# Kernel tuning notes

Hardware: AMD Instinct MI355X
Metric: run time of the kernel (lower is better)

Reference implementation:

```python
import jax, jax.numpy as jnp
import numpy as np

DIM, HID, SEQ = 768, 2048, 4096
LR, MOM, WD, THRESH = 1e-3, 0.9, 0.01, 0.1


def _net(p, x):
    W1, b1, W2, b2, W3, b3, W4, b4 = p
    h = jax.nn.relu(x @ W1 + b1)
    h = jax.nn.relu(h @ W2 + b2)
    h = jax.nn.relu(h @ W3 + b3)
    return h @ W4 + b4


def _loss(p, t):
    # t: [dim]; token.unsqueeze(0) then mse_loss (mean over all elements)
    pred = _net(p, t[None, :])
    return jnp.mean((pred - t[None, :]) ** 2)


def _ttt(params, x):
    toks = x[::4]  # `if i % 4 != 0: continue`

    def step(carry, t):
        p, buf, inited = carry
        g = jax.grad(_loss)(p, t)
        surprise = sum(jnp.linalg.norm(gi) for gi in jax.tree_util.tree_leaves(g))
        # momentum buffer: first observation initializes it
        buf_new = jnp.where(inited, MOM * buf + (1.0 - MOM) * surprise, surprise)

        def upd(q):
            qd = jax.tree_util.tree_map(lambda w: w * (1.0 - WD), q)  # weight decay
            g2 = jax.grad(_loss)(qd, t)                                # fresh fwd/bwd
            return jax.tree_util.tree_map(lambda w, gi: w - LR * gi, qd, g2)  # SGD step

        p_new = jax.lax.cond(buf_new > THRESH, upd, lambda q: q, p)
        return (p_new, buf_new, jnp.bool_(True)), None

    (pf, _, _), _ = jax.lax.scan(step, (params, jnp.float32(0.0), jnp.bool_(False)), toks)
    return pf


def setup_inputs() -> dict:
    key = jax.random.key(0)
    ks = jax.random.split(key, 5)

    def lin(k, fi, fo):
        kw, kb = jax.random.split(k)
        w = jax.random.normal(kw, (fi, fo), jnp.float32) / np.sqrt(fi).astype(np.float32)
        b = jax.random.normal(kb, (fo,), jnp.float32) * 0.01
        return w, b

    W1, b1 = lin(ks[0], DIM, HID)
    W2, b2 = lin(ks[1], HID, HID)
    W3, b3 = lin(ks[2], HID, HID)
    W4, b4 = lin(ks[3], HID, DIM)
    x = jax.random.normal(ks[4], (SEQ, DIM), jnp.float32)
    return dict(x=x, W1=W1, b1=b1, W2=W2, b2=b2, W3=W3, b3=b3, W4=W4, b4=b4, do_ttt=1)


def reference(x, W1, b1, W2, b2, W3, b3, W4, b4, do_ttt):
    params = (W1, b1, W2, b2, W3, b3, W4, b4)
    if do_ttt:
        params = _ttt(params, x)
    out = _net(params, x)            # eval pass over full sequence
    return out.mean(axis=0, keepdims=True)  # memory_summary [1, dim]
```

## Files before the change

### kernel.cpp

```cpp
#include <hip/hip_runtime.h>
#include <cstddef>

#define LRC 0.001f
#define DEC 0.99f

static const size_t OFF_Z1P = 0;
static const size_t OFF_Z2P = 65536;
static const size_t OFF_Z2Q = 131072;
static const size_t OFF_Z3P = 196608;
static const size_t OFF_Z3Q = 262144;
static const size_t OFF_Z4P = 327680;
static const size_t OFF_Z4Q = 352256;
static const size_t OFF_H1F = 376832;
static const size_t OFF_H1Q = 378880;
static const size_t OFF_H2F = 380928;
static const size_t OFF_H2Q = 382976;
static const size_t OFF_H3F = 385024;
static const size_t OFF_H3Q = 387072;
static const size_t OFF_D4F = 389120;
static const size_t OFF_D4Q = 389888;
static const size_t OFF_D3F = 390656;
static const size_t OFF_D3Q = 392704;
static const size_t OFF_D2F = 394752;
static const size_t OFF_D2Q = 396800;
static const size_t OFF_D1F = 398848;
static const size_t OFF_D1Q = 400896;
static const size_t OFF_NSQ = 402944;
static const size_t OFF_SL3 = 402960;
static const size_t OFF_SL2 = 403216;
static const size_t OFF_SL1 = 403472;
static const size_t OFF_BUF = 403728;
static const size_t OFF_MSUM = 403732;
static const size_t OFF_HA  = 428308;
static const size_t OFF_HB  = 2525460;

__device__ inline void fma4(float4& a, float s, const float4& w) {
    a.x += s * w.x; a.y += s * w.y; a.z += s * w.z; a.w += s * w.w;
}

__device__ float block_reduce_512(float v) {
    __shared__ float red[512];
    int t = threadIdx.x;
    red[t] = v;
    __syncthreads();
    for (int s = 256; s > 0; s >>= 1) {
        if (t < s) red[t] += red[t + s];
        __syncthreads();
    }
    float r = red[0];
    __syncthreads();
    return r;
}

__global__ __launch_bounds__(512) void k_fwd1(const float* __restrict__ xt,
                                              const float* __restrict__ W1,
                                              float* __restrict__ z1p,
                                              const int* __restrict__ flag) {
    if (*flag == 0) return;
    int b = blockIdx.x;
    int g = b >> 5, p = b & 31;
    int tid = threadIdx.x, w = tid >> 6, lane = tid & 63;
    int c0 = g * 256 + lane * 4;
    int kb = p * 24 + w * 3;
    float4 acc = make_float4(0.f, 0.f, 0.f, 0.f);
#pragma unroll
    for (int r = 0; r < 3; ++r) {
        float a = xt[kb + r];
        const float4 wv = *(const float4*)(W1 + (size_t)(kb + r) * 2048 + c0);
        fma4(acc, a, wv);
    }
    __shared__ float4 red[8][64];
    red[w][lane] = acc;
    __syncthreads();
    if (w == 0) {
        float4 s = red[0][lane];
#pragma unroll
        for (int q = 1; q < 8; ++q) {
            float4 r2 = red[q][lane];
            s.x += r2.x; s.y += r2.y; s.z += r2.z; s.w += r2.w;
        }
        *(float4*)(z1p + (size_t)p * 2048 + c0) = s;
    }
}

__global__ __launch_bounds__(512) void k_fwd2(const float* __restrict__ zinP,
                                              const float* __restrict__ zinQ,
                                              const float* __restrict__ bin,
                                              const float* __restrict__ W, int Nout,
                                              float* __restrict__ zoutP,
                                              float* __restrict__ zoutQ,
                                              const int* __restrict__ flag) {
    if (*flag == 0) return;
    int b = blockIdx.x;
    int g = b >> 5, p = b & 31;
    int tid = threadIdx.x, w = tid >> 6, lane = tid & 63;
    __shared__ float hs[64], hq[64];
    if (tid < 64) {
        int k = p * 64 + tid;
        float s = 0.f;
#pragma unroll 8
        for (int pp = 0; pp < 32; ++pp) s += zinP[pp * 2048 + k];
        float bv = bin[k];
        float h = fmaxf(s + bv, 0.f);
        float hqq;
        if (zinQ) {
            float sq = 0.f;
#pragma unroll 8
            for (int pp = 0; pp < 32; ++pp) sq += zinQ[pp * 2048 + k];
            hqq = fmaxf(DEC * (sq + bv), 0.f);
        } else {
            hqq = DEC * h;
        }
        hs[tid] = h; hq[tid] = hqq;
    }
    __syncthreads();
    int c0 = g * 256 + lane * 4;
    float4 ap = make_float4(0.f, 0.f, 0.f, 0.f);
    float4 aq = make_float4(0.f, 0.f, 0.f, 0.f);
#pragma unroll
    for (int r = 0; r < 8; ++r) {
        int kk = w * 8 + r;
        float a = hs[kk], a2 = hq[kk];
        const float4 wv = *(const float4*)(W + (size_t)(p * 64 + kk) * Nout + c0);
        fma4(ap, a, wv);
        fma4(aq, a2, wv);
    }
    __shared__ float4 redP[8][64];
    __shared__ float4 redQ[8][64];
    redP[w][lane] = ap; redQ[w][lane] = aq;
    __syncthreads();
    if (w == 0) {
        float4 sp = redP[0][lane], sq4 = redQ[0][lane];
#pragma unroll
        for (int q = 1; q < 8; ++q) {
            float4 r2 = redP[q][lane]; sp.x += r2.x; sp.y += r2.y; sp.z += r2.z; sp.w += r2.w;
            float4 r3 = redQ[q][lane]; sq4.x += r3.x; sq4.y += r3.y; sq4.z += r3.z; sq4.w += r3.w;
        }
        *(float4*)(zoutP + (size_t)p * Nout + c0) = sp;
        *(float4*)(zoutQ + (size_t)p * Nout + c0) = sq4;
    }
}

__global__ __launch_bounds__(512) void k_fin(float* __restrict__ wsf,
                                             const float* __restrict__ xt,
                                             const float* __restrict__ b1,
                                             const float* __restrict__ b2,
                                             const float* __restrict__ b3,
                                             const float* __restrict__ b4,
                                             const int* __restrict__ flag) {
    if (*flag == 0) return;
    int b = blockIdx.x, tid = threadIdx.x;
    if (b < 16) {
        if (tid < 128) {
            int e = b * 128 + tid;
            float s = 0.f;
#pragma unroll 8
            for (int pp = 0; pp < 32; ++pp) s += wsf[OFF_Z1P + pp * 2048 + e];
            float h = fmaxf(s + b1[e], 0.f);
            wsf[OFF_H1F + e] = h;
            wsf[OFF_H1Q + e] = DEC * h;
        }
    } else if (b < 32) {
        if (tid < 128) {
            int e = (b - 16) * 128 + tid;
            float s = 0.f, sq = 0.f;
#pragma unroll 8
            for (int pp = 0; pp < 32; ++pp) {
                s += wsf[OFF_Z2P + pp * 2048 + e];
                sq += wsf[OFF_Z2Q + pp * 2048 + e];
            }
            float bv = b2[e];
            wsf[OFF_H2F + e] = fmaxf(s + bv, 0.f);
            wsf[OFF_H2Q + e] = fmaxf(DEC * (sq + bv), 0.f);
        }
    } else if (b < 48) {
        if (tid < 128) {
            int e = (b - 32) * 128 + tid;
            float s = 0.f, sq = 0.f;
#pragma unroll 8
            for (int pp = 0; pp < 32; ++pp) {
                s += wsf[OFF_Z3P + pp * 2048 + e];
                sq += wsf[OFF_Z3Q + pp * 2048 + e];
            }
            float bv = b3[e];
            wsf[OFF_H3F + e] = fmaxf(s + bv, 0.f);
            wsf[OFF_H3Q + e] = fmaxf(DEC * (sq + bv), 0.f);
        }
    } else if (b == 48) {
        for (int e = tid; e < 768; e += 512) {
            float s = 0.f, sq = 0.f;
#pragma unroll 8
            for (int pp = 0; pp < 32; ++pp) {
                s += wsf[OFF_Z4P + pp * 768 + e];
                sq += wsf[OFF_Z4Q + pp * 768 + e];
            }
            float bv = b4[e], tv = xt[e];
            float pred = s + bv;
            float predq = DEC * (sq + bv);
            wsf[OFF_D4F + e] = 2.f * (pred - tv) * (1.f / 768.f);
            wsf[OFF_D4Q + e] = 2.f * (predq - tv) * (1.f / 768.f);
        }
    } else if (b == 49) {
        float v = 0.f;
        for (int e = tid; e < 768; e += 512) { float xv = xt[e]; v += xv * xv; }
        float s = block_reduce_512(v);
        if (tid == 0) wsf[OFF_NSQ + 0] = s;
    } else if (b == 50) {
        float v = 0.f;
        for (int e = tid; e < 2048; e += 512) {
            float s = 0.f;
#pragma unroll 8
            for (int pp = 0; pp < 32; ++pp) s += wsf[OFF_Z1P + pp * 2048 + e];
            float h = fmaxf(s + b1[e], 0.f);
            v += h * h;
        }
        float s = block_reduce_512(v);
        if (tid == 0) wsf[OFF_NSQ + 1] = s;
    } else if (b == 51) {
        float v = 0.f;
        for (int e = tid; e < 2048; e += 512) {
            float s = 0.f;
#pragma unroll 8
            for (int pp = 0; pp < 32; ++pp) s += wsf[OFF_Z2P + pp * 2048 + e];
            float h = fmaxf(s + b2[e], 0.f);
            v += h * h;
        }
        float s = block_reduce_512(v);
        if (tid == 0) wsf[OFF_NSQ + 2] = s;
    } else if (b == 52) {
        float v = 0.f;
        for (int e = tid; e < 2048; e += 512) {
            float s = 0.f;
#pragma unroll 8
            for (int pp = 0; pp < 32; ++pp) s += wsf[OFF_Z3P + pp * 2048 + e];
            float h = fmaxf(s + b3[e], 0.f);
            v += h * h;
        }
        float s = block_reduce_512(v);
        if (tid == 0) wsf[OFF_NSQ + 3] = s;
    } else if (b == 53) {
        float v = 0.f;
        for (int e = tid; e < 768; e += 512) {
            float s = 0.f;
#pragma unroll 8
            for (int pp = 0; pp < 32; ++pp) s += wsf[OFF_Z4P + pp * 768 + e];
            float d = 2.f * ((s + b4[e]) - xt[e]) * (1.f / 768.f);
            v += d * d;
        }
        float s = block_reduce_512(v);
        if (tid == 0) wsf[OFF_NSQ + 4] = s;
    }
}

__global__ __launch_bounds__(512) void k_bwd(const float* __restrict__ W, int K,
                                             const float* __restrict__ dinP,
                                             const float* __restrict__ dinQ,
                                             const float* __restrict__ hP,
                                             const float* __restrict__ hQ,
                                             float* __restrict__ doutP,
                                             float* __restrict__ doutQ,
                                             float* __restrict__ slot,
                                             const int* __restrict__ flag) {
    if (*flag == 0) return;
    __shared__ float dsP[2048];
    __shared__ float dsQ[2048];
    int tid = threadIdx.x;
    for (int k = tid; k < K; k += 512) { dsP[k] = dinP[k]; dsQ[k] = dinQ[k]; }
    __syncthreads();
    int w = tid >> 6, lane = tid & 63;
    int j = blockIdx.x * 8 + w;
    const float* row = W + (size_t)j * K;
    float ap = 0.f, aq = 0.f;
    for (int k4 = lane * 4; k4 < K; k4 += 256) {
        const float4 wv = *(const float4*)(row + k4);
        ap += wv.x * dsP[k4] + wv.y * dsP[k4 + 1] + wv.z * dsP[k4 + 2] + wv.w * dsP[k4 + 3];
        aq += wv.x * dsQ[k4] + wv.y * dsQ[k4 + 1] + wv.z * dsQ[k4 + 2] + wv.w * dsQ[k4 + 3];
    }
#pragma unroll
    for (int off = 32; off > 0; off >>= 1) {
        ap += __shfl_down(ap, off);
        aq += __shfl_down(aq, off);
    }
    __shared__ float sqw[8];
    if (lane == 0) {
        float dp = (hP[j] > 0.f) ? ap : 0.f;
        float dq = (hQ[j] > 0.f) ? DEC * aq : 0.f;
        doutP[j] = dp;
        doutQ[j] = dq;
        sqw[w] = dp * dp;
    }
    __syncthreads();
    if (tid == 0) {
        float s = 0.f;
#pragma unroll
        for (int q = 0; q < 8; ++q) s += sqw[q];
        slot[blockIdx.x] = s;
    }
}

__global__ __launch_bounds__(512) void k_upd(int step, float* __restrict__ wsf,
                                             float* __restrict__ W1, float* __restrict__ b1,
                                             float* __restrict__ W2, float* __restrict__ b2,
                                             float* __restrict__ W3, float* __restrict__ b3,
                                             float* __restrict__ W4, float* __restrict__ b4,
                                             const float* __restrict__ xt,
                                             const int* __restrict__ flag) {
    if (*flag == 0) return;
    int tid = threadIdx.x, b = blockIdx.x;
    float s3 = block_reduce_512((tid < 256) ? wsf[OFF_SL3 + tid] : 0.f);
    float s2 = block_reduce_512((tid < 256) ? wsf[OFF_SL2 + tid] : 0.f);
    float s1 = block_reduce_512((tid < 256) ? wsf[OFF_SL1 + tid] : 0.f);
    __shared__ float condsh;
    if (tid == 0) {
        float nx = sqrtf(wsf[OFF_NSQ + 0]);
        float nh1 = sqrtf(wsf[OFF_NSQ + 1]);
        float nh2 = sqrtf(wsf[OFF_NSQ + 2]);
        float nh3 = sqrtf(wsf[OFF_NSQ + 3]);
        float nd4 = sqrtf(wsf[OFF_NSQ + 4]);
        float nd3 = sqrtf(s3), nd2 = sqrtf(s2), nd1 = sqrtf(s1);
        float surprise = nx * nd1 + nd1 + nh1 * nd2 + nd2 + nh2 * nd3 + nd3 + nh3 * nd4 + nd4;
        float bufold = wsf[OFF_BUF + (step & 1)];
        float bufnew = (step == 0) ? surprise : (0.9f * bufold + 0.1f * surprise);
        wsf[OFF_BUF + ((step + 1) & 1)] = bufnew;
        condsh = (bufnew > 0.1f) ? 1.f : 0.f;
    }
    __syncthreads();
    if (condsh == 0.f) return;

    const float* d1q = wsf + OFF_D1Q;
    const float* d2q = wsf + OFF_D2Q;
    const float* d3q = wsf + OFF_D3Q;
    const float* d4q = wsf + OFF_D4Q;
    const float* h1q = wsf + OFF_H1Q;
    const float* h2q = wsf + OFF_H2Q;
    const float* h3q = wsf + OFF_H3Q;
    int c = tid * 4;
    {
        float4 dv = *(const float4*)(d1q + c);
#pragma unroll
        for (int r = 0; r < 3; ++r) {
            int i = b * 3 + r;
            float u = LRC * xt[i];
            float4* wp = (float4*)(W1 + (size_t)i * 2048 + c);
            float4 wv = *wp;
            wv.x = DEC * wv.x - u * dv.x; wv.y = DEC * wv.y - u * dv.y;
            wv.z = DEC * wv.z - u * dv.z; wv.w = DEC * wv.w - u * dv.w;
            *wp = wv;
        }
    }
    {
        float4 dv = *(const float4*)(d2q + c);
#pragma unroll
        for (int r = 0; r < 8; ++r) {
            int i = b * 8 + r;
            float u = LRC * h1q[i];
            float4* wp = (float4*)(W2 + (size_t)i * 2048 + c);
            float4 wv = *wp;
            wv.x = DEC * wv.x - u * dv.x; wv.y = DEC * wv.y - u * dv.y;
            wv.z = DEC * wv.z - u * dv.z; wv.w = DEC * wv.w - u * dv.w;
            *wp = wv;
        }
    }
    {
        float4 dv = *(const float4*)(d3q + c);
#pragma unroll
        for (int r = 0; r < 8; ++r) {
            int i = b * 8 + r;
            float u = LRC * h2q[i];
            float4* wp = (float4*)(W3 + (size_t)i * 2048 + c);
            float4 wv = *wp;
            wv.x = DEC * wv.x - u * dv.x; wv.y = DEC * wv.y - u * dv.y;
            wv.z = DEC * wv.z - u * dv.z; wv.w = DEC * wv.w - u * dv.w;
            *wp = wv;
        }
    }
    if (tid < 192) {
        float4 dv = *(const float4*)(d4q + c);
#pragma unroll
        for (int r = 0; r < 8; ++r) {
            int i = b * 8 + r;
            float u = LRC * h3q[i];
            float4* wp = (float4*)(W4 + (size_t)i * 768 + c);
            float4 wv = *wp;
            wv.x = DEC * wv.x - u * dv.x; wv.y = DEC * wv.y - u * dv.y;
            wv.z = DEC * wv.z - u * dv.z; wv.w = DEC * wv.w - u * dv.w;
            *wp = wv;
        }
    }
    if (b == 0) {
        float4 dv = *(const float4*)(d1q + c);
        float4* bp = (float4*)(b1 + c);
        float4 bv = *bp;
        bv.x = DEC * bv.x - LRC * dv.x; bv.y = DEC * bv.y - LRC * dv.y;
        bv.z = DEC * bv.z - LRC * dv.z; bv.w = DEC * bv.w - LRC * dv.w;
        *bp = bv;
    } else if (b == 1) {
        float4 dv = *(const float4*)(d2q + c);
        float4* bp = (float4*)(b2 + c);
        float4 bv = *bp;
        bv.x = DEC * bv.x - LRC * dv.x; bv.y = DEC * bv.y - LRC * dv.y;
        bv.z = DEC * bv.z - LRC * dv.z; bv.w = DEC * bv.w - LRC * dv.w;
        *bp = bv;
    } else if (b == 2) {
        float4 dv = *(const float4*)(d3q + c);
        float4* bp = (float4*)(b3 + c);
        float4 bv = *bp;
        bv.x = DEC * bv.x - LRC * dv.x; bv.y = DEC * bv.y - LRC * dv.y;
        bv.z = DEC * bv.z - LRC * dv.z; bv.w = DEC * bv.w - LRC * dv.w;
        *bp = bv;
    } else if (b == 3 && tid < 192) {
        float4 dv = *(const float4*)(d4q + c);
        float4* bp = (float4*)(b4 + c);
        float4 bv = *bp;
        bv.x = DEC * bv.x - LRC * dv.x; bv.y = DEC * bv.y - LRC * dv.y;
        bv.z = DEC * bv.z - LRC * dv.z; bv.w = DEC * bv.w - LRC * dv.w;
        *bp = bv;
    }
}

__global__ __launch_bounds__(256) void k_gemm(const float* __restrict__ A,
                                              const float* __restrict__ W,
                                              const float* __restrict__ bias,
                                              float* __restrict__ C,
                                              int M, int N, int K, int do_relu) {
    __shared__ float sA[16][64];
    __shared__ float sB[16][128];
    int bn = blockIdx.x, bm = blockIdx.y;
    int m0 = bm * 64, n0 = bn * 128;
    int tid = threadIdx.x;
    int tx = tid & 31, ty = tid >> 5;
    float acc[8][4];
#pragma unroll
    for (int i = 0; i < 8; ++i)
#pragma unroll
        for (int j = 0; j < 4; ++j) acc[i][j] = 0.f;

    for (int kt = 0; kt < K; kt += 16) {
        {
            int r = tid >> 2, cc = (tid & 3) * 4;
            const float4 a4 = *(const float4*)(A + (size_t)(m0 + r) * K + kt + cc);
            sA[cc + 0][r] = a4.x; sA[cc + 1][r] = a4.y; sA[cc + 2][r] = a4.z; sA[cc + 3][r] = a4.w;
        }
        {
            int r = tid >> 5, cc = (tid & 31) * 4;
            *(float4*)(&sB[r][cc]) = *(const float4*)(W + (size_t)(kt + r) * N + n0 + cc);
            *(float4*)(&sB[r + 8][cc]) = *(const float4*)(W + (size_t)(kt + r + 8) * N + n0 + cc);
        }
        __syncthreads();
#pragma unroll
        for (int k = 0; k < 16; ++k) {
            float av[8];
#pragma unroll
            for (int i = 0; i < 8; ++i) av[i] = sA[k][ty * 8 + i];
            float bx = sB[k][tx * 4 + 0], by = sB[k][tx * 4 + 1];
            float bz = sB[k][tx * 4 + 2], bw = sB[k][tx * 4 + 3];
#pragma unroll
            for (int i = 0; i < 8; ++i) {
                acc[i][0] += av[i] * bx; acc[i][1] += av[i] * by;
                acc[i][2] += av[i] * bz; acc[i][3] += av[i] * bw;
            }
        }
        __syncthreads();
    }
    float bx = bias[n0 + tx * 4 + 0], by = bias[n0 + tx * 4 + 1];
    float bz = bias[n0 + tx * 4 + 2], bw = bias[n0 + tx * 4 + 3];
#pragma unroll
    for (int i = 0; i < 8; ++i) {
        int m = m0 + ty * 8 + i;
        float4 v;
        v.x = acc[i][0] + bx; v.y = acc[i][1] + by;
        v.z = acc[i][2] + bz; v.w = acc[i][3] + bw;
        if (do_relu) {
            v.x = fmaxf(v.x, 0.f); v.y = fmaxf(v.y, 0.f);
            v.z = fmaxf(v.z, 0.f); v.w = fmaxf(v.w, 0.f);
        }
        *(float4*)(C + (size_t)m * N + n0 + tx * 4) = v;
    }
}

__global__ __launch_bounds__(128) void k_colsum(const float* __restrict__ Y,
                                                float* __restrict__ out) {
    int c = blockIdx.x * 128 + threadIdx.x;
    int r0 = blockIdx.y * 128;
    float s = 0.f;
    for (int r = 0; r < 128; ++r) s += Y[(size_t)(r0 + r) * 768 + c];
    out[blockIdx.y * 768 + c] = s;
}

__global__ __launch_bounds__(768) void k_out(const float* __restrict__ msum,
                                             float* __restrict__ out) {
    int c = threadIdx.x;
    float s = 0.f;
#pragma unroll
    for (int i = 0; i < 32; ++i) s += msum[i * 768 + c];
    out[c] = s * (1.f / 4096.f);
}

extern "C" void kernel_launch(void* const* d_in, const int* in_sizes, int n_in,
                              void* d_out, int out_size, void* d_ws, size_t ws_size,
                              hipStream_t stream) {
    const float* x = (const float*)d_in[0];
    float* W1 = (float*)d_in[1];
    float* b1 = (float*)d_in[2];
    float* W2 = (float*)d_in[3];
    float* b2 = (float*)d_in[4];
    float* W3 = (float*)d_in[5];
    float* b3 = (float*)d_in[6];
    float* W4 = (float*)d_in[7];
    float* b4 = (float*)d_in[8];
    const int* flag = (const int*)d_in[9];
    float* wsf = (float*)d_ws;

    for (int s = 0; s < 1024; ++s) {
        const float* xt = x + (size_t)s * 4 * 768;
        k_fwd1<<<256, 512, 0, stream>>>(xt, W1, wsf + OFF_Z1P, flag);
        k_fwd2<<<256, 512, 0, stream>>>(wsf + OFF_Z1P, nullptr, b1, W2, 2048,
                                        wsf + OFF_Z2P, wsf + OFF_Z2Q, flag);
        k_fwd2<<<256, 512, 0, stream>>>(wsf + OFF_Z2P, wsf + OFF_Z2Q, b2, W3, 2048,
                                        wsf + OFF_Z3P, wsf + OFF_Z3Q, flag);
        k_fwd2<<<96, 512, 0, stream>>>(wsf + OFF_Z3P, wsf + OFF_Z3Q, b3, W4, 768,
                                       wsf + OFF_Z4P, wsf + OFF_Z4Q, flag);
        k_fin<<<64, 512, 0, stream>>>(wsf, xt, b1, b2, b3, b4, flag);
        k_bwd<<<256, 512, 0, stream>>>(W4, 768, wsf + OFF_D4F, wsf + OFF_D4Q,
                                       wsf + OFF_H3F, wsf + OFF_H3Q,
                                       wsf + OFF_D3F, wsf + OFF_D3Q, wsf + OFF_SL3, flag);
        k_bwd<<<256, 512, 0, stream>>>(W3, 2048, wsf + OFF_D3F, wsf + OFF_D3Q,
                                       wsf + OFF_H2F, wsf + OFF_H2Q,
                                       wsf + OFF_D2F, wsf + OFF_D2Q, wsf + OFF_SL2, flag);
        k_bwd<<<256, 512, 0, stream>>>(W2, 2048, wsf + OFF_D2F, wsf + OFF_D2Q,
                                       wsf + OFF_H1F, wsf + OFF_H1Q,
                                       wsf + OFF_D1F, wsf + OFF_D1Q, wsf + OFF_SL1, flag);
        k_upd<<<256, 512, 0, stream>>>(s, wsf, W1, b1, W2, b2, W3, b3, W4, b4, xt, flag);
    }

    float* HA = wsf + OFF_HA;
    float* HB = wsf + OFF_HB;
    for (int ch = 0; ch < 4; ++ch) {
        const float* Xc = x + (size_t)ch * 1024 * 768;
        k_gemm<<<dim3(16, 16), 256, 0, stream>>>(Xc, W1, b1, HA, 1024, 2048, 768, 1);
        k_gemm<<<dim3(16, 16), 256, 0, stream>>>(HA, W2, b2, HB, 1024, 2048, 2048, 1);
        k_gemm<<<dim3(16, 16), 256, 0, stream>>>(HB, W3, b3, HA, 1024, 2048, 2048, 1);
        k_gemm<<<dim3(6, 16), 256, 0, stream>>>(HA, W4, b4, HB, 1024, 768, 2048, 0);
        k_colsum<<<dim3(6, 8), 128, 0, stream>>>(HB, wsf + OFF_MSUM + (size_t)ch * 8 * 768);
    }
    k_out<<<1, 768, 0, stream>>>(wsf + OFF_MSUM, (float*)d_out);
}
```

Baseline: 68.12 ms.

## Defer weight update into next step's forward kernels to drop per-step update pass

The per-step SGD/weight-decay update kernel is removed from the loop. Step s-1's surprise check and rank-1 weight update are instead applied lazily inside step s's forward kernels, which already read each weight tile. Each weight matrix is now read and written once per step instead of read twice, and one launch per step disappears. A final k_upd handles the last step. The cost is more complex cross-step state and a redundant surprise computation in every fwd1 block.

```diff
diff --git a/kernel.cpp b/kernel.cpp
--- a/kernel.cpp
+++ b/kernel.cpp
@@ -30,6 +30,7 @@
 static const size_t OFF_SL2 = 403216;
 static const size_t OFF_SL1 = 403472;
 static const size_t OFF_BUF = 403728;
+static const size_t OFF_CONDF = 403730;
 static const size_t OFF_MSUM = 403732;
 static const size_t OFF_HA  = 428308;
 static const size_t OFF_HB  = 2525460;
@@ -52,9 +53,12 @@
     return r;
 }
 
-__global__ __launch_bounds__(512) void k_fwd1(const float* __restrict__ xt,
-                                              const float* __restrict__ W1,
-                                              float* __restrict__ z1p,
+__global__ __launch_bounds__(512) void k_fwd1(int step,
+                                              const float* __restrict__ xt,
+                                              const float* __restrict__ xprev,
+                                              float* __restrict__ W1,
+                                              float* __restrict__ b1,
+                                              float* __restrict__ wsf,
                                               const int* __restrict__ flag) {
     if (*flag == 0) return;
     int b = blockIdx.x;
@@ -62,13 +66,70 @@
     int tid = threadIdx.x, w = tid >> 6, lane = tid & 63;
     int c0 = g * 256 + lane * 4;
     int kb = p * 24 + w * 3;
+
+    float4 wv0 = *(const float4*)(W1 + (size_t)(kb + 0) * 2048 + c0);
+    float4 wv1 = *(const float4*)(W1 + (size_t)(kb + 1) * 2048 + c0);
+    float4 wv2 = *(const float4*)(W1 + (size_t)(kb + 2) * 2048 + c0);
+    float a0 = xt[kb + 0], a1 = xt[kb + 1], a2 = xt[kb + 2];
+    float4 dv = make_float4(0.f, 0.f, 0.f, 0.f);
+    float u0 = 0.f, u1 = 0.f, u2 = 0.f;
+    if (step > 0) {
+        dv = *(const float4*)(wsf + OFF_D1Q + c0);
+        u0 = LRC * xprev[kb + 0]; u1 = LRC * xprev[kb + 1]; u2 = LRC * xprev[kb + 2];
+    }
+
+    __shared__ float cnd[4];
+    float cond = 0.f;
+    if (step > 0) {
+        if (w < 3) {
+            const float* sl = wsf + (w == 0 ? OFF_SL1 : (w == 1 ? OFF_SL2 : OFF_SL3));
+            float v = sl[lane] + sl[lane + 64] + sl[lane + 128] + sl[lane + 192];
+#pragma unroll
+            for (int off = 32; off > 0; off >>= 1) v += __shfl_down(v, off);
+            if (lane == 0) cnd[w] = v;
+        }
+        __syncthreads();
+        float nd1 = sqrtf(cnd[0]), nd2 = sqrtf(cnd[1]), nd3 = sqrtf(cnd[2]);
+        float nx = sqrtf(wsf[OFF_NSQ + 0]);
+        float nh1 = sqrtf(wsf[OFF_NSQ + 1]);
+        float nh2 = sqrtf(wsf[OFF_NSQ + 2]);
+        float nh3 = sqrtf(wsf[OFF_NSQ + 3]);
+        float nd4 = sqrtf(wsf[OFF_NSQ + 4]);
+        float surprise = nx * nd1 + nd1 + nh1 * nd2 + nd2 + nh2 * nd3 + nd3 + nh3 * nd4 + nd4;
+        float bufold = wsf[OFF_BUF + ((step - 1) & 1)];
+        float bufnew = (step == 1) ? surprise : (0.9f * bufold + 0.1f * surprise);
+        cond = (bufnew > 0.1f) ? 1.f : 0.f;
+        if (b == 0 && tid == 0) {
+            wsf[OFF_BUF + (step & 1)] = bufnew;
+            wsf[OFF_CONDF] = cond;
+        }
+    } else {
+        if (b == 0 && tid == 0) wsf[OFF_CONDF] = 0.f;
+    }
+
+    if (cond != 0.f) {
+        wv0.x = DEC * wv0.x - u0 * dv.x; wv0.y = DEC * wv0.y - u0 * dv.y;
+        wv0.z = DEC * wv0.z - u0 * dv.z; wv0.w = DEC * wv0.w - u0 * dv.w;
+        wv1.x = DEC * wv1.x - u1 * dv.x; wv1.y = DEC * wv1.y - u1 * dv.y;
+        wv1.z = DEC * wv1.z - u1 * dv.z; wv1.w = DEC * wv1.w - u1 * dv.w;
+        wv2.x = DEC * wv2.x - u2 * dv.x; wv2.y = DEC * wv2.y - u2 * dv.y;
+        wv2.z = DEC * wv2.z - u2 * dv.z; wv2.w = DEC * wv2.w - u2 * dv.w;
+        *(float4*)(W1 + (size_t)(kb + 0) * 2048 + c0) = wv0;
+        *(float4*)(W1 + (size_t)(kb + 1) * 2048 + c0) = wv1;
+        *(float4*)(W1 + (size_t)(kb + 2) * 2048 + c0) = wv2;
+        if (b == 0) {
+            int c = tid * 4;
+            float4 dq = *(const float4*)(wsf + OFF_D1Q + c);
+            float4 bv = *(float4*)(b1 + c);
+            bv.x = DEC * bv.x - LRC * dq.x; bv.y = DEC * bv.y - LRC * dq.y;
+            bv.z = DEC * bv.z - LRC * dq.z; bv.w = DEC * bv.w - LRC * dq.w;
+            *(float4*)(b1 + c) = bv;
+        }
+    }
+
     float4 acc = make_float4(0.f, 0.f, 0.f, 0.f);
-#pragma unroll
-    for (int r = 0; r < 3; ++r) {
-        float a = xt[kb + r];
-        const float4 wv = *(const float4*)(W1 + (size_t)(kb + r) * 2048 + c0);
-        fma4(acc, a, wv);
-    }
+    fma4(acc, a0, wv0); fma4(acc, a1, wv1); fma4(acc, a2, wv2);
+
     __shared__ float4 red[8][64];
     red[w][lane] = acc;
     __syncthreads();
@@ -79,22 +140,28 @@
             float4 r2 = red[q][lane];
             s.x += r2.x; s.y += r2.y; s.z += r2.z; s.w += r2.w;
         }
-        *(float4*)(z1p + (size_t)p * 2048 + c0) = s;
+        *(float4*)(wsf + OFF_Z1P + (size_t)p * 2048 + c0) = s;
     }
 }
 
 __global__ __launch_bounds__(512) void k_fwd2(const float* __restrict__ zinP,
                                               const float* __restrict__ zinQ,
                                               const float* __restrict__ bin,
-                                              const float* __restrict__ W, int Nout,
+                                              float* __restrict__ W, int Nout,
                                               float* __restrict__ zoutP,
                                               float* __restrict__ zoutQ,
+                                              const float* __restrict__ uprev,
+                                              const float* __restrict__ vprev,
+                                              float* __restrict__ bl,
+                                              const float* __restrict__ wsf,
                                               const int* __restrict__ flag) {
     if (*flag == 0) return;
     int b = blockIdx.x;
     int g = b >> 5, p = b & 31;
     int tid = threadIdx.x, w = tid >> 6, lane = tid & 63;
-    __shared__ float hs[64], hq[64];
+    bool upd = (wsf[OFF_CONDF] != 0.f);
+
+    __shared__ float hs[64], hq[64], us[64];
     if (tid < 64) {
         int k = p * 64 + tid;
         float s = 0.f;
@@ -112,18 +179,47 @@
             hqq = DEC * h;
         }
         hs[tid] = h; hq[tid] = hqq;
+        us[tid] = upd ? (LRC * uprev[k]) : 0.f;
     }
     __syncthreads();
     int c0 = g * 256 + lane * 4;
+    float4 vpv = make_float4(0.f, 0.f, 0.f, 0.f);
+    if (upd) vpv = *(const float4*)(vprev + c0);
     float4 ap = make_float4(0.f, 0.f, 0.f, 0.f);
     float4 aq = make_float4(0.f, 0.f, 0.f, 0.f);
-#pragma unroll
-    for (int r = 0; r < 8; ++r) {
-        int kk = w * 8 + r;
-        float a = hs[kk], a2 = hq[kk];
-        const float4 wv = *(const float4*)(W + (size_t)(p * 64 + kk) * Nout + c0);
-        fma4(ap, a, wv);
-        fma4(aq, a2, wv);
+    if (upd) {
+#pragma unroll
+        for (int r = 0; r < 8; ++r) {
+            int kk = w * 8 + r;
+            float* wp = W + (size_t)(p * 64 + kk) * Nout + c0;
+            float4 wv = *(const float4*)wp;
+            float u = us[kk];
+            wv.x = DEC * wv.x - u * vpv.x; wv.y = DEC * wv.y - u * vpv.y;
+            wv.z = DEC * wv.z - u * vpv.z; wv.w = DEC * wv.w - u * vpv.w;
+            *(float4*)wp = wv;
+            float a = hs[kk], a2 = hq[kk];
+            fma4(ap, a, wv);
+            fma4(aq, a2, wv);
+        }
+    } else {
+#pragma unroll
+        for (int r = 0; r < 8; ++r) {
+            int kk = w * 8 + r;
+            const float4 wv = *(const float4*)(W + (size_t)(p * 64 + kk) * Nout + c0);
+            float a = hs[kk], a2 = hq[kk];
+            fma4(ap, a, wv);
+            fma4(aq, a2, wv);
+        }
+    }
+    if (upd && b == 0) {
+        int c = tid * 4;
+        if (c < Nout) {
+            float4 dq = *(const float4*)(vprev + c);
+            float4 bv = *(float4*)(bl + c);
+            bv.x = DEC * bv.x - LRC * dq.x; bv.y = DEC * bv.y - LRC * dq.y;
+            bv.z = DEC * bv.z - LRC * dq.z; bv.w = DEC * bv.w - LRC * dq.w;
+            *(float4*)(bl + c) = bv;
+        }
     }
     __shared__ float4 redP[8][64];
     __shared__ float4 redQ[8][64];
@@ -513,13 +609,17 @@
 
     for (int s = 0; s < 1024; ++s) {
         const float* xt = x + (size_t)s * 4 * 768;
-        k_fwd1<<<256, 512, 0, stream>>>(xt, W1, wsf + OFF_Z1P, flag);
+        const float* xprev = x + (size_t)(s > 0 ? s - 1 : 0) * 4 * 768;
+        k_fwd1<<<256, 512, 0, stream>>>(s, xt, xprev, W1, b1, wsf, flag);
         k_fwd2<<<256, 512, 0, stream>>>(wsf + OFF_Z1P, nullptr, b1, W2, 2048,
-                                        wsf + OFF_Z2P, wsf + OFF_Z2Q, flag);
+                                        wsf + OFF_Z2P, wsf + OFF_Z2Q,
+                                        wsf + OFF_H1Q, wsf + OFF_D2Q, b2, wsf, flag);
         k_fwd2<<<256, 512, 0, stream>>>(wsf + OFF_Z2P, wsf + OFF_Z2Q, b2, W3, 2048,
-                                        wsf + OFF_Z3P, wsf + OFF_Z3Q, flag);
+                                        wsf + OFF_Z3P, wsf + OFF_Z3Q,
+                                        wsf + OFF_H2Q, wsf + OFF_D3Q, b3, wsf, flag);
         k_fwd2<<<96, 512, 0, stream>>>(wsf + OFF_Z3P, wsf + OFF_Z3Q, b3, W4, 768,
-                                       wsf + OFF_Z4P, wsf + OFF_Z4Q, flag);
+                                       wsf + OFF_Z4P, wsf + OFF_Z4Q,
+                                       wsf + OFF_H3Q, wsf + OFF_D4Q, b4, wsf, flag);
         k_fin<<<64, 512, 0, stream>>>(wsf, xt, b1, b2, b3, b4, flag);
         k_bwd<<<256, 512, 0, stream>>>(W4, 768, wsf + OFF_D4F, wsf + OFF_D4Q,
                                        wsf + OFF_H3F, wsf + OFF_H3Q,
@@ -530,8 +630,9 @@
         k_bwd<<<256, 512, 0, stream>>>(W2, 2048, wsf + OFF_D2F, wsf + OFF_D2Q,
                                        wsf + OFF_H1F, wsf + OFF_H1Q,
                                        wsf + OFF_D1F, wsf + OFF_D1Q, wsf + OFF_SL1, flag);
-        k_upd<<<256, 512, 0, stream>>>(s, wsf, W1, b1, W2, b2, W3, b3, W4, b4, xt, flag);
-    }
+    }
+    k_upd<<<256, 512, 0, stream>>>(1023, wsf, W1, b1, W2, b2, W3, b3, W4, b4,
+                                   x + (size_t)1023 * 4 * 768, flag);
 
     float* HA = wsf + OFF_HA;
     float* HB = wsf + OFF_HB;
```

Measured after the change: 64.39 ms. 1.06x faster.
